# Kernel optimization log

Hardware: AMD Instinct MI355X
Metric: run time of the kernel (lower is better)

Reference implementation:

```python
import jax, jax.numpy as jnp
import numpy as np

NUM_REL = 8
NUM_NODE = 100000
TYPED_NUM_NODE = 50000   # typed_num_node per relation (static)
EDGES_PER_REL = 800000   # avg degree 16
IN_C = 128
HID_C = 128


def setup_inputs() -> dict:
    key = jax.random.key(0)
    k1, k2, k3, k4, k5 = jax.random.split(key, 5)
    x = jax.random.normal(k1, (NUM_NODE, IN_C), dtype=jnp.float32)
    rel_weight = jax.random.normal(k2, (NUM_REL, IN_C, HID_C), dtype=jnp.float32) * 0.05
    sub_ptr = jnp.sort(jax.random.randint(k3, (NUM_REL, TYPED_NUM_NODE + 1), 0, EDGES_PER_REL), axis=-1)
    sub_idx = jax.random.randint(k4, (NUM_REL, EDGES_PER_REL), 0, NUM_NODE)
    sub_target = jax.random.randint(k5, (NUM_REL, TYPED_NUM_NODE), 0, NUM_NODE)
    return {"x": x, "rel_weight": rel_weight, "sub_ptr": sub_ptr,
            "sub_idx": sub_idx, "sub_target": sub_target}


def _csr_segment_ids(ptr):
    # CSR ptr [N+1] -> per-edge destination segment id [E]
    e = jnp.arange(EDGES_PER_REL)
    return jnp.clip(jnp.searchsorted(ptr, e, side='right') - 1, 0, TYPED_NUM_NODE - 1)


def reference(x, rel_weight, sub_ptr, sub_idx, sub_target):
    outs = []
    for r in range(NUM_REL):  # small fixed relation count
        seg = _csr_segment_ids(sub_ptr[r])
        # sage_sum_forward: sum neighbor features per destination node
        agg = jax.ops.segment_sum(x[sub_idx[r]], seg, num_segments=TYPED_NUM_NODE)  # [T, C]
        outs.append(agg @ rel_weight[r])  # [T, H]
    arr = jnp.concatenate(outs, axis=0)            # [R*T, H]
    tgt = sub_target.reshape(-1)                   # [R*T]
    out = jnp.zeros((NUM_NODE, HID_C), dtype=x.dtype).at[tgt].add(arr)
    return out
```

## Files before the change

kernel.cpp:

```cpp
#include <hip/hip_runtime.h>

#define NREL 8
#define NNODE 100000
#define TNODE 50000
#define NEDGE 800000
#define C 128
#define TILE_T 64
#define NTILE ((TNODE + TILE_T - 1) / TILE_T)
#define NENT (NREL * TNODE)
#define NB_SCAN ((NNODE + 255) / 256)

typedef unsigned int u32;
typedef unsigned short u16;
typedef __attribute__((ext_vector_type(8))) short bf16x8;
typedef __attribute__((ext_vector_type(4))) float f32x4;
typedef __attribute__((ext_vector_type(2))) float f32x2;

__device__ __forceinline__ float bf2f(u16 h) {
    union { u32 u; float f; } c; c.u = ((u32)h) << 16; return c.f;
}
__device__ __forceinline__ u16 f2bf(float f) {
    union { float f; u32 u; } c; c.f = f;
    u32 u = c.u + 0x7FFFu + ((c.u >> 16) & 1u);
    return (u16)(u >> 16);
}
__device__ __forceinline__ u32 pack2(float a, float b) {
    return (u32)f2bf(a) | ((u32)f2bf(b) << 16);
}
__device__ __forceinline__ float2 unpack_bf2(u32 p) {
    union { u32 u; float f; } a, b;
    a.u = p << 16; b.u = p & 0xFFFF0000u;
    return make_float2(a.f, b.f);
}
__device__ __forceinline__ f32x2 bits2(u32 p) {
    union { u32 u[2]; f32x2 f; } c;
    c.u[0] = p << 16; c.u[1] = p & 0xFFFF0000u;
    return c.f;
}
__device__ __forceinline__ void addp(f32x2* a, uint4 v) {
    a[0] += bits2(v.x); a[1] += bits2(v.y);
    a[2] += bits2(v.z); a[3] += bits2(v.w);
}
__device__ __forceinline__ void fma4(float4& acc, float a, float w0, float w1, float w2, float w3) {
    acc.x = fmaf(a, w0, acc.x);
    acc.y = fmaf(a, w1, acc.y);
    acc.z = fmaf(a, w2, acc.z);
    acc.w = fmaf(a, w3, acc.w);
}

__global__ __launch_bounds__(256)
void convert_x_kernel(const float* __restrict__ x, u16* __restrict__ xb, int n4) {
    int i = blockIdx.x * 256 + threadIdx.x;
    const int stride = gridDim.x * 256;
    for (; i < n4; i += stride) {
        const float4 v = ((const float4*)x)[i];
        ushort4 o;
        o.x = f2bf(v.x); o.y = f2bf(v.y); o.z = f2bf(v.z); o.w = f2bf(v.w);
        ((ushort4*)xb)[i] = o;
    }
}

__global__ __launch_bounds__(256)
void convert_w_kernel(const float* __restrict__ w, u16* __restrict__ wtb) {
    const int o = blockIdx.x * 256 + threadIdx.x;
    if (o < NREL * C * C) {
        const int r = o >> 14, rem = o & 16383, cc = rem >> 7, k = rem & 127;
        wtb[o] = f2bf(w[(r << 14) + k * C + cc]);
    }
}

__global__ __launch_bounds__(256)
void hist_kernel(const int* __restrict__ tgt, int* __restrict__ count) {
    const int g = blockIdx.x * 256 + threadIdx.x;
    if (g < NENT) atomicAdd(&count[tgt[g]], 1);
}

__global__ __launch_bounds__(256)
void scan1_kernel(const int* __restrict__ count, int* __restrict__ bsum) {
    __shared__ int s[256];
    const int tid = threadIdx.x;
    const int i = blockIdx.x * 256 + tid;
    s[tid] = (i < NNODE) ? count[i] : 0;
    __syncthreads();
    for (int st = 128; st > 0; st >>= 1) {
        if (tid < st) s[tid] += s[tid + st];
        __syncthreads();
    }
    if (tid == 0) bsum[blockIdx.x] = s[0];
}

__global__ __launch_bounds__(512)
void scan2_kernel(int* __restrict__ bsum) {
    __shared__ int s[512];
    const int tid = threadIdx.x;
    const int v = (tid < NB_SCAN) ? bsum[tid] : 0;
    s[tid] = v;
    __syncthreads();
    for (int st = 1; st < 512; st <<= 1) {
        const int t = (tid >= st) ? s[tid - st] : 0;
        __syncthreads();
        s[tid] += t;
        __syncthreads();
    }
    if (tid < NB_SCAN) bsum[tid] = s[tid] - v;
}

__global__ __launch_bounds__(256)
void scan3_kernel(const int* __restrict__ count, const int* __restrict__ bsum,
                  int* __restrict__ offsets, int* __restrict__ cursor) {
    __shared__ int s[256];
    const int tid = threadIdx.x;
    const int i = blockIdx.x * 256 + tid;
    const int v = (i < NNODE) ? count[i] : 0;
    s[tid] = v;
    __syncthreads();
    for (int st = 1; st < 256; st <<= 1) {
        const int t = (tid >= st) ? s[tid - st] : 0;
        __syncthreads();
        s[tid] += t;
        __syncthreads();
    }
    if (i < NNODE) {
        const int off = bsum[blockIdx.x] + s[tid] - v;
        offsets[i] = off;
        cursor[i]  = off;
    }
}

__global__ __launch_bounds__(256)
void fill_kernel(const int* __restrict__ tgt, int* __restrict__ cursor, int* __restrict__ list) {
    const int g = blockIdx.x * 256 + threadIdx.x;
    if (g < NENT) {
        const int pos = atomicAdd(&cursor[tgt[g]], 1);
        list[pos] = g;
    }
}

__global__ __launch_bounds__(512, 6)
void fused_gather_gemm_kernel(const u16* __restrict__ xb, const int* __restrict__ ptr,
                              const int* __restrict__ idx, const u16* __restrict__ wtb,
                              u16* __restrict__ P) {
    __shared__ u16 sB[C * 136];
    __shared__ u16 sA[TILE_T * 136];
    __shared__ int qcount;

    const int tid  = threadIdx.x;
    const int tile = blockIdx.x;
    const int r    = blockIdx.y;
    const int w    = tid >> 6;
    const int lane = tid & 63;

    {
        const uint4* src = (const uint4*)(wtb + (size_t)r * C * C);
        #pragma unroll
        for (int i = 0; i < 4; ++i) {
            const int f = tid + i * 512;
            const int col = f >> 4, unit = f & 15;
            *(uint4*)(sB + col * 136 + unit * 8) = src[f];
        }
    }
    if (tid == 0) qcount = 0;
    __syncthreads();

    const int* pr = ptr + r * (TNODE + 1);
    const int* er = idx + (size_t)r * NEDGE;
    const int q  = lane >> 4;
    const int sl = lane & 15;
    const u16* xcol = xb + sl * 8;

    for (;;) {
        int tl;
        if (lane == 0) tl = atomicAdd(&qcount, 1);
        tl = __shfl(tl, 0);
        if (tl >= TILE_T) break;

        const int t = tile * TILE_T + tl;
        f32x2 accA[4], accB[4];
        #pragma unroll
        for (int j = 0; j < 4; ++j) { accA[j] = (f32x2){0.f, 0.f}; accB[j] = (f32x2){0.f, 0.f}; }

        if (t < TNODE) {
            const int start = (t == 0) ? 0 : pr[t];
            const int end   = (t == TNODE - 1) ? NEDGE : pr[t + 1];

            for (int base = start; base < end; base += 64) {
                const int cnt = min(end - base, 64);
                int myi = (lane < cnt) ? er[base + lane] : 0;
                int i = 0;
                for (; i + 8 <= cnt; i += 8) {
                    const int sA0 = __shfl(myi, i + q);
                    const int sB0 = __shfl(myi, i + 4 + q);
                    const uint4 vA = *(const uint4*)(xcol + (size_t)sA0 * C);
                    const uint4 vB = *(const uint4*)(xcol + (size_t)sB0 * C);
                    addp(accA, vA);
                    addp(accB, vB);
                }
                if (i + 4 <= cnt) {
                    const int sA0 = __shfl(myi, i + q);
                    const uint4 vA = *(const uint4*)(xcol + (size_t)sA0 * C);
                    addp(accA, vA);
                    i += 4;
                }
                if (i < cnt) {
                    const int rem = cnt - i;
                    const int sA0 = __shfl(myi, i + ((q < rem) ? q : 0));
                    if (q < rem) {
                        const uint4 vA = *(const uint4*)(xcol + (size_t)sA0 * C);
                        addp(accA, vA);
                    }
                }
            }
        }
        #pragma unroll
        for (int j = 0; j < 4; ++j) {
            accA[j] += accB[j];
            accA[j].x += __shfl_xor(accA[j].x, 16);
            accA[j].y += __shfl_xor(accA[j].y, 16);
            accA[j].x += __shfl_xor(accA[j].x, 32);
            accA[j].y += __shfl_xor(accA[j].y, 32);
        }
        if (q == 0) {
            uint4 o;
            o.x = pack2(accA[0].x, accA[0].y);
            o.y = pack2(accA[1].x, accA[1].y);
            o.z = pack2(accA[2].x, accA[2].y);
            o.w = pack2(accA[3].x, accA[3].y);
            *(uint4*)(sA + tl * 136 + sl * 8) = o;
        }
    }
    __syncthreads();

    const int wr    = (w & 3) * 16;
    const int cbase = (w >> 2) * 4;
    const int fr    = lane & 15;
    const int fq    = lane >> 4;

    f32x4 acc[4];
    #pragma unroll
    for (int cf = 0; cf < 4; ++cf) acc[cf] = (f32x4){0.f, 0.f, 0.f, 0.f};

    #pragma unroll
    for (int ks = 0; ks < 4; ++ks) {
        const bf16x8 a = *(const bf16x8*)(sA + (wr + fr) * 136 + ks * 32 + fq * 8);
        #pragma unroll
        for (int cf = 0; cf < 4; ++cf) {
            const bf16x8 b = *(const bf16x8*)(sB + ((cbase + cf) * 16 + fr) * 136 + ks * 32 + fq * 8);
            acc[cf] = __builtin_amdgcn_mfma_f32_16x16x32_bf16(a, b, acc[cf], 0, 0, 0);
        }
    }
    __syncthreads();

    #pragma unroll
    for (int cf = 0; cf < 4; ++cf) {
        #pragma unroll
        for (int j = 0; j < 4; ++j) {
            const int row = wr + fq * 4 + j;
            sA[row * 136 + (cbase + cf) * 16 + fr] = f2bf(acc[cf][j]);
        }
    }
    __syncthreads();

    #pragma unroll
    for (int i = 0; i < 2; ++i) {
        const int f = tid + i * 512;
        const int row = f >> 4, unit = f & 15;
        const int t = tile * TILE_T + row;
        if (t < TNODE)
            *(uint4*)(P + ((size_t)r * TNODE + t) * C + unit * 8) =
                *(const uint4*)(sA + row * 136 + unit * 8);
    }
}

__global__ __launch_bounds__(256)
void out_gather_kernel(const u16* __restrict__ P, const int* __restrict__ offsets,
                       const int* __restrict__ count, const int* __restrict__ list,
                       float* __restrict__ out) {
    const int lane = threadIdx.x & 63;
    const int n = blockIdx.x * 4 + (threadIdx.x >> 6);
    if (n >= NNODE) return;
    const int st = offsets[n];
    const int en = st + count[n];
    float2 a0 = make_float2(0.f, 0.f), a1 = make_float2(0.f, 0.f);
    int i = st;
    for (; i + 2 <= en; i += 2) {
        const u32 v0 = ((const u32*)(P + (size_t)list[i] * C))[lane];
        const u32 v1 = ((const u32*)(P + (size_t)list[i + 1] * C))[lane];
        const float2 f0 = unpack_bf2(v0), f1 = unpack_bf2(v1);
        a0.x += f0.x; a0.y += f0.y;
        a1.x += f1.x; a1.y += f1.y;
    }
    if (i < en) {
        const float2 f0 = unpack_bf2(((const u32*)(P + (size_t)list[i] * C))[lane]);
        a0.x += f0.x; a0.y += f0.y;
    }
    a0.x += a1.x; a0.y += a1.y;
    ((float2*)(out + (size_t)n * C))[lane] = a0;
}

__device__ __forceinline__ void add4(float4& acc, const float4& b) {
    acc.x += b.x; acc.y += b.y; acc.z += b.z; acc.w += b.w;
}
__global__ __launch_bounds__(256, 1)
void rgcn_fused_kernel(const float* __restrict__ x, const float* __restrict__ w,
                       const int* __restrict__ ptr, const int* __restrict__ idx,
                       const int* __restrict__ tgt, float* __restrict__ out) {
    __shared__ float sW[C * C];
    __shared__ float sAgg[TILE_T][C + 4];
    const int tid = threadIdx.x, tile = blockIdx.x, r = blockIdx.y;
    {
        const float4* src = (const float4*)(w + (size_t)r * C * C);
        float4* dst = (float4*)sW;
        #pragma unroll
        for (int i = 0; i < 16; ++i) dst[tid + i * 256] = src[tid + i * 256];
    }
    {
        const int tl = tid >> 2, g = tid & 3;
        const int t = tile * TILE_T + tl;
        float4 a[8];
        #pragma unroll
        for (int j = 0; j < 8; ++j) a[j] = make_float4(0.f, 0.f, 0.f, 0.f);
        if (t < TNODE) {
            const int* pr = ptr + (size_t)r * (TNODE + 1);
            const int* er = idx + (size_t)r * NEDGE;
            int e = (t == 0) ? 0 : pr[t];
            const int end = (t == TNODE - 1) ? NEDGE : pr[t + 1];
            for (; e < end; ++e) {
                const int s0 = er[e];
                const float4* r0 = (const float4*)(x + (size_t)s0 * C) + g * 8;
                #pragma unroll
                for (int j = 0; j < 8; ++j) add4(a[j], r0[j]);
            }
        }
        float* rowp = &sAgg[tl][g * 32];
        #pragma unroll
        for (int j = 0; j < 8; ++j) ((float4*)rowp)[j] = a[j];
    }
    __syncthreads();
    const int tg = tid >> 4, cg = tid & 15;
    float4 acc0[4], acc1[4];
    #pragma unroll
    for (int i = 0; i < 4; ++i) {
        acc0[i] = make_float4(0.f, 0.f, 0.f, 0.f);
        acc1[i] = make_float4(0.f, 0.f, 0.f, 0.f);
    }
    for (int k4 = 0; k4 < C / 4; ++k4) {
        float4 av[4];
        #pragma unroll
        for (int i = 0; i < 4; ++i) av[i] = *(const float4*)&sAgg[tg * 4 + i][k4 * 4];
        #pragma unroll
        for (int kk = 0; kk < 4; ++kk) {
            const int k = k4 * 4 + kk;
            const float4 w0 = *(const float4*)&sW[k * C + cg * 4];
            const float4 w1 = *(const float4*)&sW[k * C + 64 + cg * 4];
            #pragma unroll
            for (int i = 0; i < 4; ++i) {
                const float a = ((const float*)&av[i])[kk];
                fma4(acc0[i], a, w0.x, w0.y, w0.z, w0.w);
                fma4(acc1[i], a, w1.x, w1.y, w1.z, w1.w);
            }
        }
    }
    const int* tr = tgt + (size_t)r * TNODE;
    #pragma unroll
    for (int i = 0; i < 4; ++i) {
        const int t = tile * TILE_T + tg * 4 + i;
        if (t < TNODE) {
            const int node = tr[t];
            float* ob = out + (size_t)node * C + cg * 4;
            unsafeAtomicAdd(ob + 0, acc0[i].x);  unsafeAtomicAdd(ob + 1, acc0[i].y);
            unsafeAtomicAdd(ob + 2, acc0[i].z);  unsafeAtomicAdd(ob + 3, acc0[i].w);
            unsafeAtomicAdd(ob + 64, acc1[i].x); unsafeAtomicAdd(ob + 65, acc1[i].y);
            unsafeAtomicAdd(ob + 66, acc1[i].z); unsafeAtomicAdd(ob + 67, acc1[i].w);
        }
    }
}

extern "C" void kernel_launch(void* const* d_in, const int* in_sizes, int n_in,
                              void* d_out, int out_size, void* d_ws, size_t ws_size,
                              hipStream_t stream) {
    const float* x   = (const float*)d_in[0];
    const float* w   = (const float*)d_in[1];
    const int*   ptr = (const int*)d_in[2];
    const int*   idx = (const int*)d_in[3];
    const int*   tgt = (const int*)d_in[4];
    float* out = (float*)d_out;

    const size_t P_OFF    = 0;
    const size_t XB_OFF   = 104000000;
    const size_t WTB_OFF  = 130000000;
    const size_t CNT_OFF  = 131000000;
    const size_t OFFS_OFF = 131500000;
    const size_t CUR_OFF  = 132000000;
    const size_t BSUM_OFF = 132500000;
    const size_t LIST_OFF = 133000000;
    const size_t WS_NEED  = 135000000;

    if (ws_size >= WS_NEED) {
        char* base = (char*)d_ws;
        u16*   P       = (u16*)(base + P_OFF);
        u16*   xb      = (u16*)(base + XB_OFF);
        u16*   wtb     = (u16*)(base + WTB_OFF);
        int*   count   = (int*)(base + CNT_OFF);
        int*   offsets = (int*)(base + OFFS_OFF);
        int*   cursor  = (int*)(base + CUR_OFF);
        int*   bsum    = (int*)(base + BSUM_OFF);
        int*   list    = (int*)(base + LIST_OFF);

        convert_x_kernel<<<2048, 256, 0, stream>>>(x, xb, NNODE * C / 4);
        convert_w_kernel<<<(NREL * C * C + 255) / 256, 256, 0, stream>>>(w, wtb);

        hipMemsetAsync(count, 0, NNODE * sizeof(int), stream);
        hist_kernel<<<(NENT + 255) / 256, 256, 0, stream>>>(tgt, count);
        scan1_kernel<<<NB_SCAN, 256, 0, stream>>>(count, bsum);
        scan2_kernel<<<1, 512, 0, stream>>>(bsum);
        scan3_kernel<<<NB_SCAN, 256, 0, stream>>>(count, bsum, offsets, cursor);
        fill_kernel<<<(NENT + 255) / 256, 256, 0, stream>>>(tgt, cursor, list);

        dim3 grid(NTILE, NREL);
        fused_gather_gemm_kernel<<<grid, 512, 0, stream>>>(xb, ptr, idx, wtb, P);

        out_gather_kernel<<<(NNODE + 3) / 4, 256, 0, stream>>>(P, offsets, count, list, out);
    } else {
        hipMemsetAsync(out, 0, (size_t)NNODE * C * sizeof(float), stream);
        dim3 grid(NTILE, NREL);
        rgcn_fused_kernel<<<grid, 256, 0, stream>>>(x, w, ptr, idx, tgt, out);
    }
}
```

Before: 345.6 us.

## Shard bf16 features by channel and split gather from MFMA GEMM

Converts x into eight channel-sharded bf16 copies (16 channels each), so each gather block touches only one 3.2MB shard. The goal is to improve L2 hit rates during the random neighbour gather. The fused gather+GEMM kernel is split into a sharded gather that writes aggregated features to a workspace and a separate MFMA GEMM kernel that reads them back. This adds an extra round trip through global memory for the aggregates and needs a larger workspace, falling back to the old path if the workspace is too small.

```diff
diff --git a/kernel.cpp b/kernel.cpp
--- a/kernel.cpp
+++ b/kernel.cpp
@@ -9,6 +9,7 @@
 #define NTILE ((TNODE + TILE_T - 1) / TILE_T)
 #define NENT (NREL * TNODE)
 #define NB_SCAN ((NNODE + 255) / 256)
+#define NSHARD 8
 
 typedef unsigned int u32;
 typedef unsigned short u16;
@@ -16,9 +17,6 @@
 typedef __attribute__((ext_vector_type(4))) float f32x4;
 typedef __attribute__((ext_vector_type(2))) float f32x2;
 
-__device__ __forceinline__ float bf2f(u16 h) {
-    union { u32 u; float f; } c; c.u = ((u32)h) << 16; return c.f;
-}
 __device__ __forceinline__ u16 f2bf(float f) {
     union { float f; u32 u; } c; c.f = f;
     u32 u = c.u + 0x7FFFu + ((c.u >> 16) & 1u);
@@ -46,6 +44,24 @@
     acc.y = fmaf(a, w1, acc.y);
     acc.z = fmaf(a, w2, acc.z);
     acc.w = fmaf(a, w3, acc.w);
+}
+
+__global__ __launch_bounds__(256)
+void convert_x_shard_kernel(const float* __restrict__ x, u16* __restrict__ xbS) {
+    int j = blockIdx.x * 256 + threadIdx.x;
+    if (j >= NSHARD * NNODE) return;
+    const int sh = j / NNODE;
+    const int node = j - sh * NNODE;
+    const float4* src = (const float4*)(x + (size_t)node * C + sh * 16);
+    u16* dst = xbS + (size_t)j * 16;
+    #pragma unroll
+    for (int h = 0; h < 2; ++h) {
+        const float4 v0 = src[h * 2], v1 = src[h * 2 + 1];
+        uint4 o;
+        o.x = pack2(v0.x, v0.y); o.y = pack2(v0.z, v0.w);
+        o.z = pack2(v1.x, v1.y); o.w = pack2(v1.z, v1.w);
+        *(uint4*)(dst + h * 8) = o;
+    }
 }
 
 __global__ __launch_bounds__(256)
@@ -136,6 +152,159 @@
     }
 }
 
+__global__ __launch_bounds__(256)
+void gather_shard_kernel(const u16* __restrict__ xbS, const int* __restrict__ ptr,
+                         const int* __restrict__ idx, u16* __restrict__ aggS) {
+    const int b    = blockIdx.x;
+    const int sh   = b & 7;
+    const int item = b >> 3;
+    const int rel  = item / NTILE;
+    const int tile = item - rel * NTILE;
+
+    const int lane = threadIdx.x & 63;
+    const int w    = threadIdx.x >> 6;
+    const int grp  = lane >> 3;
+    const int c    = lane & 7;
+
+    const int* pr = ptr + rel * (TNODE + 1);
+    const int* er = idx + (size_t)rel * NEDGE;
+    const u16* xs = xbS + (size_t)sh * NNODE * 16 + c * 2;
+    u16* as = aggS + (size_t)sh * NENT * 16;
+
+    #pragma unroll
+    for (int half = 0; half < 2; ++half) {
+        const int tl = w * 16 + half * 8 + grp;
+        const int t  = tile * TILE_T + tl;
+        if (t >= TNODE) continue;
+        int s        = (t == 0) ? 0 : pr[t];
+        const int e1 = (t == TNODE - 1) ? NEDGE : pr[t + 1];
+
+        f32x2 a0 = (f32x2){0.f, 0.f}, a1 = (f32x2){0.f, 0.f};
+        for (; s + 4 <= e1; s += 4) {
+            const int i0 = er[s], i1 = er[s + 1], i2 = er[s + 2], i3 = er[s + 3];
+            const u32 v0 = *(const u32*)(xs + (size_t)i0 * 16);
+            const u32 v1 = *(const u32*)(xs + (size_t)i1 * 16);
+            const u32 v2 = *(const u32*)(xs + (size_t)i2 * 16);
+            const u32 v3 = *(const u32*)(xs + (size_t)i3 * 16);
+            a0 += bits2(v0); a1 += bits2(v1);
+            a0 += bits2(v2); a1 += bits2(v3);
+        }
+        for (; s < e1; ++s) {
+            const u32 v0 = *(const u32*)(xs + (size_t)er[s] * 16);
+            a0 += bits2(v0);
+        }
+        a0 += a1;
+
+        const int g = rel * TNODE + t;
+        *(u32*)(as + (size_t)g * 16 + c * 2) = pack2(a0.x, a0.y);
+    }
+}
+
+__global__ __launch_bounds__(256, 3)
+void gemm_mfma_kernel(const u16* __restrict__ aggS, const u16* __restrict__ wtb,
+                      u16* __restrict__ P) {
+    __shared__ u16 sB[C * 136];
+    __shared__ u16 sA[TILE_T * 136];
+
+    const int tid  = threadIdx.x;
+    const int tile = blockIdx.x;
+    const int r    = blockIdx.y;
+
+    {
+        const uint4* src = (const uint4*)(wtb + (size_t)r * C * C);
+        #pragma unroll
+        for (int i = 0; i < 8; ++i) {
+            const int f = tid + i * 256;
+            const int col = f >> 4, unit = f & 15;
+            *(uint4*)(sB + col * 136 + unit * 8) = src[f];
+        }
+    }
+    {
+        #pragma unroll
+        for (int k = 0; k < 2; ++k) {
+            const int u = tid + k * 256;
+            const int row = u >> 3, sh = u & 7;
+            const int t = tile * TILE_T + row;
+            u16* dst = sA + row * 136 + sh * 16;
+            if (t < TNODE) {
+                const u16* src = aggS + ((size_t)sh * NENT + (size_t)r * TNODE + t) * 16;
+                *(uint4*)dst       = *(const uint4*)src;
+                *(uint4*)(dst + 8) = *(const uint4*)(src + 8);
+            } else {
+                *(uint4*)dst       = make_uint4(0u, 0u, 0u, 0u);
+                *(uint4*)(dst + 8) = make_uint4(0u, 0u, 0u, 0u);
+            }
+        }
+    }
+    __syncthreads();
+
+    const int lane = tid & 63;
+    const int wr   = (tid >> 6) * 16;
+    const int fr   = lane & 15;
+    const int fq   = lane >> 4;
+
+    f32x4 acc[8];
+    #pragma unroll
+    for (int cf = 0; cf < 8; ++cf) acc[cf] = (f32x4){0.f, 0.f, 0.f, 0.f};
+
+    #pragma unroll
+    for (int ks = 0; ks < 4; ++ks) {
+        const bf16x8 a = *(const bf16x8*)(sA + (wr + fr) * 136 + ks * 32 + fq * 8);
+        #pragma unroll
+        for (int cf = 0; cf < 8; ++cf) {
+            const bf16x8 b = *(const bf16x8*)(sB + (cf * 16 + fr) * 136 + ks * 32 + fq * 8);
+            acc[cf] = __builtin_amdgcn_mfma_f32_16x16x32_bf16(a, b, acc[cf], 0, 0, 0);
+        }
+    }
+    __syncthreads();
+
+    #pragma unroll
+    for (int cf = 0; cf < 8; ++cf) {
+        #pragma unroll
+        for (int j = 0; j < 4; ++j) {
+            const int row = wr + fq * 4 + j;
+            sA[row * 136 + cf * 16 + fr] = f2bf(acc[cf][j]);
+        }
+    }
+    __syncthreads();
+
+    #pragma unroll
+    for (int i = 0; i < 4; ++i) {
+        const int f = tid + i * 256;
+        const int row = f >> 4, unit = f & 15;
+        const int t = tile * TILE_T + row;
+        if (t < TNODE)
+            *(uint4*)(P + ((size_t)r * TNODE + t) * C + unit * 8) =
+                *(const uint4*)(sA + row * 136 + unit * 8);
+    }
+}
+
+__global__ __launch_bounds__(256)
+void out_gather_kernel(const u16* __restrict__ P, const int* __restrict__ offsets,
+                       const int* __restrict__ count, const int* __restrict__ list,
+                       float* __restrict__ out) {
+    const int lane = threadIdx.x & 63;
+    const int n = blockIdx.x * 4 + (threadIdx.x >> 6);
+    if (n >= NNODE) return;
+    const int st = offsets[n];
+    const int en = st + count[n];
+    float2 a0 = make_float2(0.f, 0.f), a1 = make_float2(0.f, 0.f);
+    int i = st;
+    for (; i + 2 <= en; i += 2) {
+        const u32 v0 = ((const u32*)(P + (size_t)list[i] * C))[lane];
+        const u32 v1 = ((const u32*)(P + (size_t)list[i + 1] * C))[lane];
+        const float2 f0 = unpack_bf2(v0), f1 = unpack_bf2(v1);
+        a0.x += f0.x; a0.y += f0.y;
+        a1.x += f1.x; a1.y += f1.y;
+    }
+    if (i < en) {
+        const float2 f0 = unpack_bf2(((const u32*)(P + (size_t)list[i] * C))[lane]);
+        a0.x += f0.x; a0.y += f0.y;
+    }
+    a0.x += a1.x; a0.y += a1.y;
+    ((float2*)(out + (size_t)n * C))[lane] = a0;
+}
+
 __global__ __launch_bounds__(512, 6)
 void fused_gather_gemm_kernel(const u16* __restrict__ xb, const int* __restrict__ ptr,
                               const int* __restrict__ idx, const u16* __restrict__ wtb,
@@ -182,7 +351,6 @@
         if (t < TNODE) {
             const int start = (t == 0) ? 0 : pr[t];
             const int end   = (t == TNODE - 1) ? NEDGE : pr[t + 1];
-
             for (int base = start; base < end; base += 64) {
                 const int cnt = min(end - base, 64);
                 int myi = (lane < cnt) ? er[base + lane] : 0;
@@ -271,32 +439,6 @@
     }
 }
 
-__global__ __launch_bounds__(256)
-void out_gather_kernel(const u16* __restrict__ P, const int* __restrict__ offsets,
-                       const int* __restrict__ count, const int* __restrict__ list,
-                       float* __restrict__ out) {
-    const int lane = threadIdx.x & 63;
-    const int n = blockIdx.x * 4 + (threadIdx.x >> 6);
-    if (n >= NNODE) return;
-    const int st = offsets[n];
-    const int en = st + count[n];
-    float2 a0 = make_float2(0.f, 0.f), a1 = make_float2(0.f, 0.f);
-    int i = st;
-    for (; i + 2 <= en; i += 2) {
-        const u32 v0 = ((const u32*)(P + (size_t)list[i] * C))[lane];
-        const u32 v1 = ((const u32*)(P + (size_t)list[i + 1] * C))[lane];
-        const float2 f0 = unpack_bf2(v0), f1 = unpack_bf2(v1);
-        a0.x += f0.x; a0.y += f0.y;
-        a1.x += f1.x; a1.y += f1.y;
-    }
-    if (i < en) {
-        const float2 f0 = unpack_bf2(((const u32*)(P + (size_t)list[i] * C))[lane]);
-        a0.x += f0.x; a0.y += f0.y;
-    }
-    a0.x += a1.x; a0.y += a1.y;
-    ((float2*)(out + (size_t)n * C))[lane] = a0;
-}
-
 __device__ __forceinline__ void add4(float4& acc, const float4& b) {
     acc.x += b.x; acc.y += b.y; acc.z += b.z; acc.w += b.w;
 }
@@ -386,27 +528,31 @@
     float* out = (float*)d_out;
 
     const size_t P_OFF    = 0;
-    const size_t XB_OFF   = 104000000;
-    const size_t WTB_OFF  = 130000000;
-    const size_t CNT_OFF  = 131000000;
-    const size_t OFFS_OFF = 131500000;
-    const size_t CUR_OFF  = 132000000;
-    const size_t BSUM_OFF = 132500000;
-    const size_t LIST_OFF = 133000000;
-    const size_t WS_NEED  = 135000000;
-
-    if (ws_size >= WS_NEED) {
-        char* base = (char*)d_ws;
-        u16*   P       = (u16*)(base + P_OFF);
-        u16*   xb      = (u16*)(base + XB_OFF);
-        u16*   wtb     = (u16*)(base + WTB_OFF);
-        int*   count   = (int*)(base + CNT_OFF);
-        int*   offsets = (int*)(base + OFFS_OFF);
-        int*   cursor  = (int*)(base + CUR_OFF);
-        int*   bsum    = (int*)(base + BSUM_OFF);
-        int*   list    = (int*)(base + LIST_OFF);
-
-        convert_x_kernel<<<2048, 256, 0, stream>>>(x, xb, NNODE * C / 4);
+    const size_t AGGS_OFF = 102400000;
+    const size_t XBS_OFF  = 204800000;
+    const size_t WTB_OFF  = 230400000;
+    const size_t CNT_OFF  = 230662144;
+    const size_t OFFS_OFF = 231062144;
+    const size_t CUR_OFF  = 231462144;
+    const size_t BSUM_OFF = 231862144;
+    const size_t LIST_OFF = 231864192;
+    const size_t WS_T1    = 233464192;
+    const size_t WS_T2    = 135000000;
+
+    char* base = (char*)d_ws;
+
+    if (ws_size >= WS_T1) {
+        u16* P       = (u16*)(base + P_OFF);
+        u16* aggS    = (u16*)(base + AGGS_OFF);
+        u16* xbS     = (u16*)(base + XBS_OFF);
+        u16* wtb     = (u16*)(base + WTB_OFF);
+        int* count   = (int*)(base + CNT_OFF);
+        int* offsets = (int*)(base + OFFS_OFF);
+        int* cursor  = (int*)(base + CUR_OFF);
+        int* bsum    = (int*)(base + BSUM_OFF);
+        int* list    = (int*)(base + LIST_OFF);
+
+        convert_x_shard_kernel<<<(NSHARD * NNODE + 255) / 256, 256, 0, stream>>>(x, xbS);
         convert_w_kernel<<<(NREL * C * C + 255) / 256, 256, 0, stream>>>(w, wtb);
 
         hipMemsetAsync(count, 0, NNODE * sizeof(int), stream);
@@ -416,6 +562,32 @@
         scan3_kernel<<<NB_SCAN, 256, 0, stream>>>(count, bsum, offsets, cursor);
         fill_kernel<<<(NENT + 255) / 256, 256, 0, stream>>>(tgt, cursor, list);
 
+        gather_shard_kernel<<<NTILE * NREL * NSHARD, 256, 0, stream>>>(xbS, ptr, idx, aggS);
+
+        dim3 grid(NTILE, NREL);
+        gemm_mfma_kernel<<<grid, 256, 0, stream>>>(aggS, wtb, P);
+
+        out_gather_kernel<<<(NNODE + 3) / 4, 256, 0, stream>>>(P, offsets, count, list, out);
+    } else if (ws_size >= WS_T2) {
+        u16* P       = (u16*)(base + 0);
+        u16* xb      = (u16*)(base + 104000000);
+        u16* wtb     = (u16*)(base + 130000000);
+        int* count   = (int*)(base + 131000000);
+        int* offsets = (int*)(base + 131500000);
+        int* cursor  = (int*)(base + 132000000);
+        int* bsum    = (int*)(base + 132500000);
+        int* list    = (int*)(base + 133000000);
+
+        convert_x_kernel<<<2048, 256, 0, stream>>>(x, xb, NNODE * C / 4);
+        convert_w_kernel<<<(NREL * C * C + 255) / 256, 256, 0, stream>>>(w, wtb);
+
+        hipMemsetAsync(count, 0, NNODE * sizeof(int), stream);
+        hist_kernel<<<(NENT + 255) / 256, 256, 0, stream>>>(tgt, count);
+        scan1_kernel<<<NB_SCAN, 256, 0, stream>>>(count, bsum);
+        scan2_kernel<<<1, 512, 0, stream>>>(bsum);
+        scan3_kernel<<<NB_SCAN, 256, 0, stream>>>(count, bsum, offsets, cursor);
+        fill_kernel<<<(NENT + 255) / 256, 256, 0, stream>>>(tgt, cursor, list);
+
         dim3 grid(NTILE, NREL);
         fused_gather_gemm_kernel<<<grid, 512, 0, stream>>>(xb, ptr, idx, wtb, P);
 
```

Measured after the change: 683.9 us. 1.98x slower.

## Drop LDS weight staging, merge scan passes, raise gather-GEMM occupancy

Applied to the files above, without the earlier changes.

The fused gather-GEMM kernel no longer copies the relation weight into shared memory. It reads B fragments straight from global/L2, which frees about 34 KB of LDS and lets the launch bound ask for 8 waves per SIMD. The three-pass scan becomes two passes: scan1 writes block-local offsets, and fill and out_gather add the block prefix from bsum when they use them, so one launch and one pass over count go away. The risk is that each wave now issues repeated global loads for the weights during the MFMA loop, and the higher occupancy target may cause register spilling.

```diff
diff --git a/kernel.cpp b/kernel.cpp
--- a/kernel.cpp
+++ b/kernel.cpp
@@ -16,9 +16,6 @@
 typedef __attribute__((ext_vector_type(4))) float f32x4;
 typedef __attribute__((ext_vector_type(2))) float f32x2;
 
-__device__ __forceinline__ float bf2f(u16 h) {
-    union { u32 u; float f; } c; c.u = ((u32)h) << 16; return c.f;
-}
 __device__ __forceinline__ u16 f2bf(float f) {
     union { float f; u32 u; } c; c.f = f;
     u32 u = c.u + 0x7FFFu + ((c.u >> 16) & 1u);
@@ -76,17 +73,26 @@
 }
 
 __global__ __launch_bounds__(256)
-void scan1_kernel(const int* __restrict__ count, int* __restrict__ bsum) {
+void scan1_kernel(const int* __restrict__ count, int* __restrict__ bsum,
+                  int* __restrict__ offsets, int* __restrict__ cursor) {
     __shared__ int s[256];
     const int tid = threadIdx.x;
     const int i = blockIdx.x * 256 + tid;
-    s[tid] = (i < NNODE) ? count[i] : 0;
-    __syncthreads();
-    for (int st = 128; st > 0; st >>= 1) {
-        if (tid < st) s[tid] += s[tid + st];
+    const int v = (i < NNODE) ? count[i] : 0;
+    s[tid] = v;
+    __syncthreads();
+    for (int st = 1; st < 256; st <<= 1) {
+        const int t = (tid >= st) ? s[tid - st] : 0;
         __syncthreads();
-    }
-    if (tid == 0) bsum[blockIdx.x] = s[0];
+        s[tid] += t;
+        __syncthreads();
+    }
+    if (i < NNODE) {
+        const int loc = s[tid] - v;
+        offsets[i] = loc;
+        cursor[i]  = loc;
+    }
+    if (tid == 255) bsum[blockIdx.x] = s[255];
 }
 
 __global__ __launch_bounds__(512)
@@ -106,41 +112,20 @@
 }
 
 __global__ __launch_bounds__(256)
-void scan3_kernel(const int* __restrict__ count, const int* __restrict__ bsum,
-                  int* __restrict__ offsets, int* __restrict__ cursor) {
-    __shared__ int s[256];
-    const int tid = threadIdx.x;
-    const int i = blockIdx.x * 256 + tid;
-    const int v = (i < NNODE) ? count[i] : 0;
-    s[tid] = v;
-    __syncthreads();
-    for (int st = 1; st < 256; st <<= 1) {
-        const int t = (tid >= st) ? s[tid - st] : 0;
-        __syncthreads();
-        s[tid] += t;
-        __syncthreads();
-    }
-    if (i < NNODE) {
-        const int off = bsum[blockIdx.x] + s[tid] - v;
-        offsets[i] = off;
-        cursor[i]  = off;
-    }
-}
-
-__global__ __launch_bounds__(256)
-void fill_kernel(const int* __restrict__ tgt, int* __restrict__ cursor, int* __restrict__ list) {
+void fill_kernel(const int* __restrict__ tgt, int* __restrict__ cursor,
+                 const int* __restrict__ bsum, int* __restrict__ list) {
     const int g = blockIdx.x * 256 + threadIdx.x;
     if (g < NENT) {
-        const int pos = atomicAdd(&cursor[tgt[g]], 1);
+        const int t = tgt[g];
+        const int pos = atomicAdd(&cursor[t], 1) + bsum[t >> 8];
         list[pos] = g;
     }
 }
 
-__global__ __launch_bounds__(512, 6)
+__global__ __launch_bounds__(512, 8)
 void fused_gather_gemm_kernel(const u16* __restrict__ xb, const int* __restrict__ ptr,
                               const int* __restrict__ idx, const u16* __restrict__ wtb,
                               u16* __restrict__ P) {
-    __shared__ u16 sB[C * 136];
     __shared__ u16 sA[TILE_T * 136];
     __shared__ int qcount;
 
@@ -150,15 +135,6 @@
     const int w    = tid >> 6;
     const int lane = tid & 63;
 
-    {
-        const uint4* src = (const uint4*)(wtb + (size_t)r * C * C);
-        #pragma unroll
-        for (int i = 0; i < 4; ++i) {
-            const int f = tid + i * 512;
-            const int col = f >> 4, unit = f & 15;
-            *(uint4*)(sB + col * 136 + unit * 8) = src[f];
-        }
-    }
     if (tid == 0) qcount = 0;
     __syncthreads();
 
@@ -234,6 +210,7 @@
     const int cbase = (w >> 2) * 4;
     const int fr    = lane & 15;
     const int fq    = lane >> 4;
+    const u16* wb   = wtb + (size_t)r * C * C;
 
     f32x4 acc[4];
     #pragma unroll
@@ -244,7 +221,7 @@
         const bf16x8 a = *(const bf16x8*)(sA + (wr + fr) * 136 + ks * 32 + fq * 8);
         #pragma unroll
         for (int cf = 0; cf < 4; ++cf) {
-            const bf16x8 b = *(const bf16x8*)(sB + ((cbase + cf) * 16 + fr) * 136 + ks * 32 + fq * 8);
+            const bf16x8 b = *(const bf16x8*)(wb + ((cbase + cf) * 16 + fr) * C + ks * 32 + fq * 8);
             acc[cf] = __builtin_amdgcn_mfma_f32_16x16x32_bf16(a, b, acc[cf], 0, 0, 0);
         }
     }
@@ -273,12 +250,12 @@
 
 __global__ __launch_bounds__(256)
 void out_gather_kernel(const u16* __restrict__ P, const int* __restrict__ offsets,
-                       const int* __restrict__ count, const int* __restrict__ list,
-                       float* __restrict__ out) {
+                       const int* __restrict__ count, const int* __restrict__ bsum,
+                       const int* __restrict__ list, float* __restrict__ out) {
     const int lane = threadIdx.x & 63;
     const int n = blockIdx.x * 4 + (threadIdx.x >> 6);
     if (n >= NNODE) return;
-    const int st = offsets[n];
+    const int st = offsets[n] + bsum[n >> 8];
     const int en = st + count[n];
     float2 a0 = make_float2(0.f, 0.f), a1 = make_float2(0.f, 0.f);
     int i = st;
@@ -385,41 +362,32 @@
     const int*   tgt = (const int*)d_in[4];
     float* out = (float*)d_out;
 
-    const size_t P_OFF    = 0;
-    const size_t XB_OFF   = 104000000;
-    const size_t WTB_OFF  = 130000000;
-    const size_t CNT_OFF  = 131000000;
-    const size_t OFFS_OFF = 131500000;
-    const size_t CUR_OFF  = 132000000;
-    const size_t BSUM_OFF = 132500000;
-    const size_t LIST_OFF = 133000000;
-    const size_t WS_NEED  = 135000000;
+    const size_t WS_NEED = 135000000;
+    char* base = (char*)d_ws;
 
     if (ws_size >= WS_NEED) {
-        char* base = (char*)d_ws;
-        u16*   P       = (u16*)(base + P_OFF);
-        u16*   xb      = (u16*)(base + XB_OFF);
-        u16*   wtb     = (u16*)(base + WTB_OFF);
-        int*   count   = (int*)(base + CNT_OFF);
-        int*   offsets = (int*)(base + OFFS_OFF);
-        int*   cursor  = (int*)(base + CUR_OFF);
-        int*   bsum    = (int*)(base + BSUM_OFF);
-        int*   list    = (int*)(base + LIST_OFF);
+        u16* P       = (u16*)(base + 0);
+        u16* xb      = (u16*)(base + 104000000);
+        u16* wtb     = (u16*)(base + 130000000);
+        int* count   = (int*)(base + 131000000);
+        int* offsets = (int*)(base + 131500000);
+        int* cursor  = (int*)(base + 132000000);
+        int* bsum    = (int*)(base + 132500000);
+        int* list    = (int*)(base + 133000000);
 
         convert_x_kernel<<<2048, 256, 0, stream>>>(x, xb, NNODE * C / 4);
         convert_w_kernel<<<(NREL * C * C + 255) / 256, 256, 0, stream>>>(w, wtb);
 
         hipMemsetAsync(count, 0, NNODE * sizeof(int), stream);
         hist_kernel<<<(NENT + 255) / 256, 256, 0, stream>>>(tgt, count);
-        scan1_kernel<<<NB_SCAN, 256, 0, stream>>>(count, bsum);
+        scan1_kernel<<<NB_SCAN, 256, 0, stream>>>(count, bsum, offsets, cursor);
         scan2_kernel<<<1, 512, 0, stream>>>(bsum);
-        scan3_kernel<<<NB_SCAN, 256, 0, stream>>>(count, bsum, offsets, cursor);
-        fill_kernel<<<(NENT + 255) / 256, 256, 0, stream>>>(tgt, cursor, list);
+        fill_kernel<<<(NENT + 255) / 256, 256, 0, stream>>>(tgt, cursor, bsum, list);
 
         dim3 grid(NTILE, NREL);
         fused_gather_gemm_kernel<<<grid, 512, 0, stream>>>(xb, ptr, idx, wtb, P);
 
-        out_gather_kernel<<<(NNODE + 3) / 4, 256, 0, stream>>>(P, offsets, count, list, out);
+        out_gather_kernel<<<(NNODE + 3) / 4, 256, 0, stream>>>(P, offsets, count, bsum, list, out);
     } else {
         hipMemsetAsync(out, 0, (size_t)NNODE * C * sizeof(float), stream);
         dim3 grid(NTILE, NREL);
```

After: 368.1 us. +6.5%, slower.
